# Kernel optimization log

Measured on AMD Instinct MI355X. Metric: run time of the kernel, lower is better.

The kernel has to match this reference:

```python
import jax, jax.numpy as jnp
import numpy as np

N = 1024            # number of proposals (128 proposals x 8 images)
D_APP = 2048        # appearance feature dim
D_K = 128           # key/query/value dim
D_G = 128           # geometric embedding dim


def setup_inputs() -> dict:
    key = jax.random.key(0)
    ks = jax.random.split(key, 10)
    s_app = 1.0 / np.sqrt(D_APP)
    s_geo = 1.0 / np.sqrt(D_G)
    return {
        "app_feature": jax.random.normal(ks[0], (N, D_APP), jnp.float32),
        "position_embedding": jax.random.normal(ks[1], (N, N, D_G), jnp.float32),
        "WQ_w": jax.random.normal(ks[2], (D_K, D_APP), jnp.float32) * s_app,
        "WQ_b": jax.random.normal(ks[3], (D_K,), jnp.float32) * 0.01,
        "WK_w": jax.random.normal(ks[4], (D_K, D_APP), jnp.float32) * s_app,
        "WK_b": jax.random.normal(ks[5], (D_K,), jnp.float32) * 0.01,
        "WV_w": jax.random.normal(ks[6], (D_K, D_APP), jnp.float32) * s_app,
        "WV_b": jax.random.normal(ks[7], (D_K,), jnp.float32) * 0.01,
        "WG_w": jax.random.normal(ks[8], (1, D_G), jnp.float32) * s_geo,
        "WG_b": jax.random.normal(ks[9], (1,), jnp.float32) * 0.01,
    }


def reference(app_feature, position_embedding,
              WQ_w, WQ_b, WK_w, WK_b, WV_w, WV_b, WG_w, WG_b):
    n = app_feature.shape[0]
    dim_k = WQ_w.shape[0]
    # projections: (N, D_K)
    w_q = app_feature @ WQ_w.T + WQ_b
    w_k = app_feature @ WK_w.T + WK_b
    w_v = app_feature @ WV_w.T + WV_b
    # appearance scores: (N, N)
    scaled_dot = (w_q @ w_k.T) / jnp.sqrt(jnp.asarray(dim_k, app_feature.dtype))
    # geometric bias: Linear(D_G -> 1) + ReLU, reshaped to (N, N)
    w_g = jax.nn.relu(jnp.einsum('mng,g->mn', position_embedding, WG_w[0]) + WG_b[0])
    # additive bias then row-softmax
    w_mn = jax.nn.softmax(scaled_dot + w_g, axis=1)
    return w_mn @ w_v  # (N, D_K)
```

## Files before the change

kernel.cpp:

```cpp
#include <hip/hip_runtime.h>
#include <hip/hip_bf16.h>
#include <math.h>

#define N_PROP 1024
#define DAPP   2048
#define DK     128

__global__ __launch_bounds__(256) void init_bias_kernel(
    const float* __restrict__ bQ, const float* __restrict__ bK,
    const float* __restrict__ bV,
    float* __restrict__ Q, float* __restrict__ K, float* __restrict__ V) {
  int i = blockIdx.x * 256 + threadIdx.x;
  if (i < N_PROP * DK) {
    int c = i & (DK - 1);
    Q[i] = bQ[c];
    K[i] = bK[c];
    V[i] = bV[c];
  }
}

#define BM 64
#define BN 64
#define KC 32
#define KSPLIT_CHUNK 512

__global__ __launch_bounds__(256) void proj_kernel(
    const float* __restrict__ X,
    const float* __restrict__ WQ, const float* __restrict__ WK,
    const float* __restrict__ WV,
    float* __restrict__ Q, float* __restrict__ K, float* __restrict__ V) {
  __shared__ __attribute__((aligned(16))) float As[KC][BM + 4];
  __shared__ __attribute__((aligned(16))) float Bs[KC][BN + 4];

  const int nt = blockIdx.x;
  const int mt = blockIdx.y;
  const int kz = blockIdx.z;
  const int row0 = mt * BM;
  const int proj = nt >> 1;
  const int col0 = (nt & 1) * 64;

  const float* __restrict__ W = (proj == 0) ? WQ : ((proj == 1) ? WK : WV);
  float* __restrict__ O = (proj == 0) ? Q : ((proj == 1) ? K : V);

  const int t  = threadIdx.x;
  const int tx = t & 15, ty = t >> 4;
  const int kk = t & 31, mm = t >> 5;

  float acc[4][4] = {};

  const int k0base = kz * KSPLIT_CHUNK;
  for (int k0 = k0base; k0 < k0base + KSPLIT_CHUNK; k0 += KC) {
    __syncthreads();
#pragma unroll
    for (int r = 0; r < 8; ++r) {
      As[kk][mm + r * 8] = X[(size_t)(row0 + mm + r * 8) * DAPP + k0 + kk];
      Bs[kk][mm + r * 8] = W[(size_t)(col0 + mm + r * 8) * DAPP + k0 + kk];
    }
    __syncthreads();
#pragma unroll
    for (int k = 0; k < KC; ++k) {
      float4 a = *(const float4*)&As[k][ty * 4];
      float4 b = *(const float4*)&Bs[k][tx * 4];
      acc[0][0] += a.x * b.x; acc[0][1] += a.x * b.y; acc[0][2] += a.x * b.z; acc[0][3] += a.x * b.w;
      acc[1][0] += a.y * b.x; acc[1][1] += a.y * b.y; acc[1][2] += a.y * b.z; acc[1][3] += a.y * b.w;
      acc[2][0] += a.z * b.x; acc[2][1] += a.z * b.y; acc[2][2] += a.z * b.z; acc[2][3] += a.z * b.w;
      acc[3][0] += a.w * b.x; acc[3][1] += a.w * b.y; acc[3][2] += a.w * b.z; acc[3][3] += a.w * b.w;
    }
  }

#pragma unroll
  for (int i = 0; i < 4; ++i)
#pragma unroll
    for (int j = 0; j < 4; ++j)
      atomicAdd(&O[(size_t)(row0 + ty * 4 + i) * DK + col0 + tx * 4 + j],
                acc[i][j]);
}

__global__ __launch_bounds__(256) void score_kernel(
    const float* __restrict__ Q, const float* __restrict__ Kmat,
    float* __restrict__ S) {
  __shared__ __attribute__((aligned(16))) float As[KC][BM + 4];
  __shared__ __attribute__((aligned(16))) float Bs[KC][BN + 4];

  const int col0 = blockIdx.x * BN;
  const int row0 = blockIdx.y * BM;
  const int t  = threadIdx.x;
  const int tx = t & 15, ty = t >> 4;
  const int kk = t & 31, mm = t >> 5;

  float acc[4][4] = {};

  for (int k0 = 0; k0 < DK; k0 += KC) {
    __syncthreads();
#pragma unroll
    for (int r = 0; r < 8; ++r) {
      As[kk][mm + r * 8] = Q[(size_t)(row0 + mm + r * 8) * DK + k0 + kk];
      Bs[kk][mm + r * 8] = Kmat[(size_t)(col0 + mm + r * 8) * DK + k0 + kk];
    }
    __syncthreads();
#pragma unroll
    for (int k = 0; k < KC; ++k) {
      float4 a = *(const float4*)&As[k][ty * 4];
      float4 b = *(const float4*)&Bs[k][tx * 4];
      acc[0][0] += a.x * b.x; acc[0][1] += a.x * b.y; acc[0][2] += a.x * b.z; acc[0][3] += a.x * b.w;
      acc[1][0] += a.y * b.x; acc[1][1] += a.y * b.y; acc[1][2] += a.y * b.z; acc[1][3] += a.y * b.w;
      acc[2][0] += a.z * b.x; acc[2][1] += a.z * b.y; acc[2][2] += a.z * b.z; acc[2][3] += a.z * b.w;
      acc[3][0] += a.w * b.x; acc[3][1] += a.w * b.y; acc[3][2] += a.w * b.z; acc[3][3] += a.w * b.w;
    }
  }

  const float scale = 0.08838834764831845f;
#pragma unroll
  for (int i = 0; i < 4; ++i)
#pragma unroll
    for (int j = 0; j < 4; ++j)
      S[(size_t)(row0 + ty * 4 + i) * N_PROP + col0 + tx * 4 + j] =
          acc[i][j] * scale;
}

__global__ __launch_bounds__(256) void fused_row_kernel(
    const float* __restrict__ pos, const float* __restrict__ S,
    const float* __restrict__ V, const float* __restrict__ wg,
    const float* __restrict__ bg, float* __restrict__ out) {
  __shared__ __attribute__((aligned(16))) float logits[N_PROP];
  __shared__ __attribute__((aligned(16))) float wgs[DK];
  __shared__ __attribute__((aligned(16))) float red[256];
  __shared__ float wred[4];

  const int m = blockIdx.x;
  const int t = threadIdx.x;

  if (t < DK) wgs[t] = wg[t];
  __syncthreads();

  const int hw = t >> 5;
  const int l  = t & 31;
  const float4 w4 = *(const float4*)&wgs[l * 4];
  const float bG = bg[0];
  const float* __restrict__ posrow = pos + (size_t)m * N_PROP * DK;
  const float* __restrict__ Srow   = S + (size_t)m * N_PROP;

  for (int it = 0; it < 128; ++it) {
    const int n = it * 8 + hw;
    const float4 p4 = *(const float4*)(posrow + (size_t)n * DK + l * 4);
    float d = p4.x * w4.x + p4.y * w4.y + p4.z * w4.z + p4.w * w4.w;
#pragma unroll
    for (int off = 16; off; off >>= 1) d += __shfl_xor(d, off, 64);
    if (l == 0) {
      float g = d + bG;
      g = g > 0.0f ? g : 0.0f;
      logits[n] = Srow[n] + g;
    }
  }
  __syncthreads();

  float mx = -INFINITY;
  for (int n = t; n < N_PROP; n += 256) mx = fmaxf(mx, logits[n]);
#pragma unroll
  for (int off = 32; off; off >>= 1) mx = fmaxf(mx, __shfl_xor(mx, off, 64));
  if ((t & 63) == 0) wred[t >> 6] = mx;
  __syncthreads();
  mx = fmaxf(fmaxf(wred[0], wred[1]), fmaxf(wred[2], wred[3]));
  __syncthreads();

  float sum = 0.0f;
  for (int n = t; n < N_PROP; n += 256) {
    float e = __expf(logits[n] - mx);
    logits[n] = e;
    sum += e;
  }
#pragma unroll
  for (int off = 32; off; off >>= 1) sum += __shfl_xor(sum, off, 64);
  if ((t & 63) == 0) wred[t >> 6] = sum;
  __syncthreads();
  sum = wred[0] + wred[1] + wred[2] + wred[3];
  const float inv = 1.0f / sum;

  const int d    = t & 127;
  const int half = t >> 7;
  float acc = 0.0f;
#pragma unroll 8
  for (int n = half; n < N_PROP; n += 2)
    acc += logits[n] * V[(size_t)n * DK + d];
  red[t] = acc;
  __syncthreads();
  if (t < DK) out[(size_t)m * DK + t] = (red[t] + red[t + DK]) * inv;
}

extern "C" void kernel_launch(void* const* d_in, const int* in_sizes, int n_in,
                              void* d_out, int out_size, void* d_ws,
                              size_t ws_size, hipStream_t stream) {
  const float* app = (const float*)d_in[0];
  const float* pos = (const float*)d_in[1];
  const float* WQw = (const float*)d_in[2];
  const float* WQb = (const float*)d_in[3];
  const float* WKw = (const float*)d_in[4];
  const float* WKb = (const float*)d_in[5];
  const float* WVw = (const float*)d_in[6];
  const float* WVb = (const float*)d_in[7];
  const float* WGw = (const float*)d_in[8];
  const float* WGb = (const float*)d_in[9];
  float* out = (float*)d_out;

  float* ws = (float*)d_ws;
  float* Q = ws;
  float* K = ws + 131072;
  float* V = ws + 262144;
  float* S = ws + 393216;

  init_bias_kernel<<<dim3(512), dim3(256), 0, stream>>>(WQb, WKb, WVb, Q, K, V);

  proj_kernel<<<dim3(6, 16, 4), dim3(256), 0, stream>>>(app, WQw, WKw, WVw,
                                                        Q, K, V);

  score_kernel<<<dim3(16, 16), dim3(256), 0, stream>>>(Q, K, S);

  fused_row_kernel<<<dim3(1024), dim3(256), 0, stream>>>(pos, S, V, WGw, WGb,
                                                         out);
}
```

Baseline: 819.5 us.

## Split fused row kernel into streaming bias pass and vectorized softmax-PV kernel

Replaces the per-row fused kernel with two kernels. The first is a grid-stride geometric-bias kernel that streams the 512MB position embedding with 2048 blocks and adds ReLU(pos·wg+b) into S in place. The second does the softmax and P·V using float4 loads of S and V, with an 8-way split over n and a shared-memory reduction. The split decouples the bandwidth-bound embedding read from the softmax, at the cost of an extra launch and an extra round trip of S through global memory.

New measurement: 814.4 us. No clear change (-0.6%).

```diff
diff --git a/kernel.cpp b/kernel.cpp
--- a/kernel.cpp
+++ b/kernel.cpp
@@ -118,73 +118,82 @@
           acc[i][j] * scale;
 }
 
-__global__ __launch_bounds__(256) void fused_row_kernel(
-    const float* __restrict__ pos, const float* __restrict__ S,
-    const float* __restrict__ V, const float* __restrict__ wg,
-    const float* __restrict__ bg, float* __restrict__ out) {
-  __shared__ __attribute__((aligned(16))) float logits[N_PROP];
-  __shared__ __attribute__((aligned(16))) float wgs[DK];
-  __shared__ __attribute__((aligned(16))) float red[256];
-  __shared__ float wred[4];
-
-  const int m = blockIdx.x;
-  const int t = threadIdx.x;
-
-  if (t < DK) wgs[t] = wg[t];
-  __syncthreads();
-
+__global__ __launch_bounds__(256) void bias_kernel(
+    const float* __restrict__ pos, float* __restrict__ S,
+    const float* __restrict__ wg, const float* __restrict__ bg) {
+  const int t  = threadIdx.x;
+  const int l  = t & 31;
   const int hw = t >> 5;
-  const int l  = t & 31;
-  const float4 w4 = *(const float4*)&wgs[l * 4];
+
+  const float4 w4 = *(const float4*)&wg[l * 4];
   const float bG = bg[0];
-  const float* __restrict__ posrow = pos + (size_t)m * N_PROP * DK;
-  const float* __restrict__ Srow   = S + (size_t)m * N_PROP;
-
-  for (int it = 0; it < 128; ++it) {
-    const int n = it * 8 + hw;
-    const float4 p4 = *(const float4*)(posrow + (size_t)n * DK + l * 4);
+
+  const size_t total  = (size_t)N_PROP * N_PROP;
+  const size_t stride = (size_t)gridDim.x * 8;
+  for (size_t row = (size_t)blockIdx.x * 8 + hw; row < total; row += stride) {
+    const float4 p4 = *(const float4*)(pos + row * DK + (l << 2));
     float d = p4.x * w4.x + p4.y * w4.y + p4.z * w4.z + p4.w * w4.w;
 #pragma unroll
     for (int off = 16; off; off >>= 1) d += __shfl_xor(d, off, 64);
     if (l == 0) {
       float g = d + bG;
-      g = g > 0.0f ? g : 0.0f;
-      logits[n] = Srow[n] + g;
-    }
-  }
-  __syncthreads();
-
-  float mx = -INFINITY;
-  for (int n = t; n < N_PROP; n += 256) mx = fmaxf(mx, logits[n]);
+      S[row] += g > 0.0f ? g : 0.0f;
+    }
+  }
+}
+
+__global__ __launch_bounds__(256) void softmax_pv_kernel(
+    const float* __restrict__ S, const float* __restrict__ V,
+    float* __restrict__ out) {
+  __shared__ __attribute__((aligned(16))) float p[N_PROP];
+  __shared__ __attribute__((aligned(16))) float4 accs[256];
+  __shared__ float wred[4];
+
+  const int m = blockIdx.x;
+  const int t = threadIdx.x;
+  const float* __restrict__ Srow = S + (size_t)m * N_PROP;
+
+  const float4 s4 = ((const float4*)Srow)[t];
+  float mx = fmaxf(fmaxf(s4.x, s4.y), fmaxf(s4.z, s4.w));
 #pragma unroll
   for (int off = 32; off; off >>= 1) mx = fmaxf(mx, __shfl_xor(mx, off, 64));
   if ((t & 63) == 0) wred[t >> 6] = mx;
   __syncthreads();
   mx = fmaxf(fmaxf(wred[0], wred[1]), fmaxf(wred[2], wred[3]));
-  __syncthreads();
-
-  float sum = 0.0f;
-  for (int n = t; n < N_PROP; n += 256) {
-    float e = __expf(logits[n] - mx);
-    logits[n] = e;
-    sum += e;
-  }
+
+  const float e0 = __expf(s4.x - mx), e1 = __expf(s4.y - mx);
+  const float e2 = __expf(s4.z - mx), e3 = __expf(s4.w - mx);
+  ((float4*)p)[t] = make_float4(e0, e1, e2, e3);
+  float sum = e0 + e1 + e2 + e3;
 #pragma unroll
   for (int off = 32; off; off >>= 1) sum += __shfl_xor(sum, off, 64);
+  __syncthreads();
   if ((t & 63) == 0) wred[t >> 6] = sum;
   __syncthreads();
   sum = wred[0] + wred[1] + wred[2] + wred[3];
   const float inv = 1.0f / sum;
 
-  const int d    = t & 127;
-  const int half = t >> 7;
-  float acc = 0.0f;
-#pragma unroll 8
-  for (int n = half; n < N_PROP; n += 2)
-    acc += logits[n] * V[(size_t)n * DK + d];
-  red[t] = acc;
-  __syncthreads();
-  if (t < DK) out[(size_t)m * DK + t] = (red[t] + red[t + DK]) * inv;
+  const int dq = (t & 31) << 2;
+  const int ng = t >> 5;
+  float4 acc = make_float4(0.f, 0.f, 0.f, 0.f);
+  for (int n = ng; n < N_PROP; n += 8) {
+    const float pw = p[n];
+    const float4 v4 = *(const float4*)&V[(size_t)n * DK + dq];
+    acc.x += pw * v4.x; acc.y += pw * v4.y;
+    acc.z += pw * v4.z; acc.w += pw * v4.w;
+  }
+  accs[t] = acc;
+  __syncthreads();
+  if (t < 32) {
+    float4 r = accs[t];
+#pragma unroll
+    for (int g = 1; g < 8; ++g) {
+      const float4 o = accs[t + g * 32];
+      r.x += o.x; r.y += o.y; r.z += o.z; r.w += o.w;
+    }
+    r.x *= inv; r.y *= inv; r.z *= inv; r.w *= inv;
+    *(float4*)&out[(size_t)m * DK + (t << 2)] = r;
+  }
 }
 
 extern "C" void kernel_launch(void* const* d_in, const int* in_sizes, int n_in,
@@ -215,6 +224,7 @@
 
   score_kernel<<<dim3(16, 16), dim3(256), 0, stream>>>(Q, K, S);
 
-  fused_row_kernel<<<dim3(1024), dim3(256), 0, stream>>>(pos, S, V, WGw, WGb,
-                                                         out);
-}
+  bias_kernel<<<dim3(2048), dim3(256), 0, stream>>>(pos, S, WGw, WGb);
+
+  softmax_pv_kernel<<<dim3(1024), dim3(256), 0, stream>>>(S, V, out);
+}
```
